# Performance work log

Hardware: AMD Instinct MI355X
Metric: run time of the kernel (lower is better)

## Reference

```python
import jax, jax.numpy as jnp
import numpy as np

PATCH = 16
B, C, H, W = 4, 3, 512, 512
N = 4096  # patches per image


def setup_inputs() -> dict:
    key = jax.random.key(0)
    k1, k2, k3, k4 = jax.random.split(key, 4)
    fuse = jax.random.normal(k1, (B, C, H, W), jnp.float32)
    img1 = jax.random.normal(k2, (B, C, H, W), jnp.float32)
    img2 = jax.random.normal(k3, (B, C, H, W), jnp.float32)
    # valid top-left (h, w) so h+PATCH <= H, w+PATCH <= W
    coords = jax.random.randint(k4, (B, N, 2), 0, H - PATCH + 1, dtype=jnp.int32)
    return {"fuse": fuse, "img1": img1, "img2": img2, "coords": coords}


def _extract_patches(image, coords):
    # image: [B,C,H,W], coords: [B,N,2] -> patches [B,C,N,P] with P=PATCH*PATCH
    c = image.shape[1]

    def one(img_b, hw):
        p = jax.lax.dynamic_slice(img_b, (0, hw[0], hw[1]), (c, PATCH, PATCH))
        return p.reshape(c, PATCH * PATCH)

    pat = jax.vmap(jax.vmap(one, in_axes=(None, 0)), in_axes=(0, 0))(image, coords)  # [B,N,C,P]
    return jnp.transpose(pat, (0, 2, 1, 3))  # [B,C,N,P]


def reference(fuse, img1, img2, coords):
    pf = _extract_patches(fuse, coords)
    p1 = _extract_patches(img1, coords)
    p2 = _extract_patches(img2, coords)
    mu1 = jnp.mean(p1, axis=-1, keepdims=True)
    mu2 = jnp.mean(p2, axis=-1, keepdims=True)
    sd1 = jnp.sqrt(jnp.mean((p1 - mu1) ** 2, axis=-1, keepdims=True))
    sd2 = jnp.sqrt(jnp.mean((p2 - mu2) ** 2, axis=-1, keepdims=True))
    denom = sd1 + sd2 + 1e-6
    target = (sd1 / denom) * p1 + (sd2 / denom) * p2
    return jnp.mean(jnp.abs(pf - target))
```

## Files before the change

kernel.cpp:

```cpp
#include <hip/hip_runtime.h>

#define BD 4
#define CD 3
#define HD 512
#define WD 512
#define NPAT 4096
#define NP (BD * NPAT)
#define PLANE (HD * WD)
#define PPW 2
#define PPB (PPW * 4)
#define NBLK (NP / PPB)
#define TOTAL_ELEMS (4.0 * 3.0 * 4096.0 * 256.0)
#define CSTRIDE 260

typedef float f4 __attribute__((ext_vector_type(4), aligned(4)));

template <int CTRL>
__device__ __forceinline__ float dpp_add(float x) {
    int y = __builtin_amdgcn_update_dpp(0, __float_as_int(x), CTRL, 0xF, 0xF, true);
    return x + __int_as_float(y);
}

__device__ __forceinline__ float wave_sum64(float x) {
    x = dpp_add<0xB1>(x);
    x = dpp_add<0x4E>(x);
    x = dpp_add<0x124>(x);
    x = dpp_add<0x128>(x);
    x += __shfl_xor(x, 16, 64);
    x += __shfl_xor(x, 32, 64);
    return x;
}

__global__ __launch_bounds__(256) void build_order(
    const int* __restrict__ coords, unsigned int* __restrict__ order)
{
    __shared__ unsigned char  cnt[256 * CSTRIDE];
    __shared__ unsigned short total[256];
    __shared__ unsigned int   base[256];

    const int t = threadIdx.x;
    const int b = blockIdx.x;

    {
        unsigned int* row = (unsigned int*)(cnt + t * CSTRIDE);
        #pragma unroll
        for (int k = 0; k < CSTRIDE / 4; ++k) row[k] = 0u;
    }
    __syncthreads();

    const int2* c2 = (const int2*)coords;
    unsigned int  pk[16];
    unsigned char kk[16];
    #pragma unroll
    for (int i = 0; i < 16; ++i) {
        const int p = (b << 12) + (i << 8) + t;
        const int2 hw = c2[p];
        pk[i] = ((unsigned)b << 18) | ((unsigned)hw.x << 9) | (unsigned)hw.y;
        kk[i] = (unsigned char)(((hw.x >> 5) << 4) | (hw.y >> 5));
        cnt[t * CSTRIDE + kk[i]]++;
    }
    __syncthreads();

    {
        unsigned int run = 0;
        for (int tt = 0; tt < 256; ++tt) {
            const unsigned int v = cnt[tt * CSTRIDE + t];
            cnt[tt * CSTRIDE + t] = (unsigned char)run;
            run += v;
        }
        total[t] = (unsigned short)run;
    }
    __syncthreads();

    if (t < 64) {
        const unsigned int t0 = total[4 * t],     t1 = total[4 * t + 1];
        const unsigned int t2 = total[4 * t + 2], t3 = total[4 * t + 3];
        const unsigned int lsum = t0 + t1 + t2 + t3;
        unsigned int x = lsum;
        #pragma unroll
        for (int d = 1; d < 64; d <<= 1) {
            const unsigned int v = __shfl_up(x, d, 64);
            if (t >= d) x += v;
        }
        const unsigned int excl = x - lsum;
        base[4 * t]     = excl;
        base[4 * t + 1] = excl + t0;
        base[4 * t + 2] = excl + t0 + t1;
        base[4 * t + 3] = excl + t0 + t1 + t2;
    }
    __syncthreads();

    #pragma unroll
    for (int i = 0; i < 16; ++i) {
        const int key = kk[i];
        const unsigned int pos = base[key] + cnt[t * CSTRIDE + key];
        cnt[t * CSTRIDE + key]++;
        order[(b << 12) + pos] = pk[i];
    }
}

__global__ __launch_bounds__(256) void patch_stage1(
    const float* __restrict__ fuse,
    const float* __restrict__ img1,
    const float* __restrict__ img2,
    const unsigned int* __restrict__ order,
    float* __restrict__ partials)
{
    const int lane = threadIdx.x & 63;
    const int wave = threadIdx.x >> 6;
    const int bid  = blockIdx.x;
    const int slot0 = (((bid & 7) * (NBLK / 8) + (bid >> 3)) << 3) + wave * PPW;

    const uint2 ord = *(const uint2*)(order + slot0);

    const int wA = ord.x & 511, hA = (ord.x >> 9) & 511, bA = ord.x >> 18;
    const int wB = ord.y & 511, hB = (ord.y >> 9) & 511, bB = ord.y >> 18;

    const int roff = (lane >> 2) * WD + (lane & 3) * 4;
    const size_t baseA = ((size_t)(bA * CD) * HD + hA) * WD + wA + roff;
    const size_t baseB = ((size_t)(bB * CD) * HD + hB) * WD + wB + roff;

    f4 vfA[3], v1A[3], v2A[3], vfB[3], v1B[3], v2B[3];
    #pragma unroll
    for (int c = 0; c < CD; ++c) {
        vfA[c] = *(const f4*)(fuse + baseA + (size_t)c * PLANE);
        v1A[c] = *(const f4*)(img1 + baseA + (size_t)c * PLANE);
        v2A[c] = *(const f4*)(img2 + baseA + (size_t)c * PLANE);
        vfB[c] = *(const f4*)(fuse + baseB + (size_t)c * PLANE);
        v1B[c] = *(const f4*)(img1 + baseB + (size_t)c * PLANE);
        v2B[c] = *(const f4*)(img2 + baseB + (size_t)c * PLANE);
    }

    float s1[2][3], q1[2][3], s2[2][3], q2[2][3];
    #pragma unroll
    for (int c = 0; c < CD; ++c) {
        s1[0][c] = v1A[c].x + v1A[c].y + v1A[c].z + v1A[c].w;
        q1[0][c] = v1A[c].x*v1A[c].x + v1A[c].y*v1A[c].y + v1A[c].z*v1A[c].z + v1A[c].w*v1A[c].w;
        s2[0][c] = v2A[c].x + v2A[c].y + v2A[c].z + v2A[c].w;
        q2[0][c] = v2A[c].x*v2A[c].x + v2A[c].y*v2A[c].y + v2A[c].z*v2A[c].z + v2A[c].w*v2A[c].w;
        s1[1][c] = v1B[c].x + v1B[c].y + v1B[c].z + v1B[c].w;
        q1[1][c] = v1B[c].x*v1B[c].x + v1B[c].y*v1B[c].y + v1B[c].z*v1B[c].z + v1B[c].w*v1B[c].w;
        s2[1][c] = v2B[c].x + v2B[c].y + v2B[c].z + v2B[c].w;
        q2[1][c] = v2B[c].x*v2B[c].x + v2B[c].y*v2B[c].y + v2B[c].z*v2B[c].z + v2B[c].w*v2B[c].w;
    }

    #pragma unroll
    for (int u = 0; u < 2; ++u) {
        #pragma unroll
        for (int c = 0; c < CD; ++c) {
            s1[u][c] = wave_sum64(s1[u][c]);
            q1[u][c] = wave_sum64(q1[u][c]);
            s2[u][c] = wave_sum64(s2[u][c]);
            q2[u][c] = wave_sum64(q2[u][c]);
        }
    }

    const float inv = 1.f / 256.f;
    float acc = 0.f;
    #pragma unroll
    for (int u = 0; u < 2; ++u) {
        #pragma unroll
        for (int c = 0; c < CD; ++c) {
            const float mu1 = s1[u][c] * inv;
            const float mu2 = s2[u][c] * inv;
            const float sd1 = sqrtf(fmaxf(q1[u][c] * inv - mu1 * mu1, 0.f));
            const float sd2 = sqrtf(fmaxf(q2[u][c] * inv - mu2 * mu2, 0.f));
            const float denom = sd1 + sd2 + 1e-6f;
            const float w1 = sd1 / denom;
            const float w2 = sd2 / denom;
            const f4 vf = u ? vfB[c] : vfA[c];
            const f4 v1 = u ? v1B[c] : v1A[c];
            const f4 v2 = u ? v2B[c] : v2A[c];
            acc += fabsf(vf.x - (w1 * v1.x + w2 * v2.x))
                 + fabsf(vf.y - (w1 * v1.y + w2 * v2.y))
                 + fabsf(vf.z - (w1 * v1.z + w2 * v2.z))
                 + fabsf(vf.w - (w1 * v1.w + w2 * v2.w));
        }
    }

    acc = wave_sum64(acc);

    __shared__ float partsm[4];
    if (lane == 0) partsm[wave] = acc;
    __syncthreads();
    if (threadIdx.x == 0)
        partials[bid] = partsm[0] + partsm[1] + partsm[2] + partsm[3];
}

__global__ __launch_bounds__(256) void patch_stage2(
    const float* __restrict__ partials, float* __restrict__ out)
{
    float s = 0.f;
    for (int i = threadIdx.x; i < NBLK; i += 256)
        s += partials[i];

    s = wave_sum64(s);

    __shared__ float partsm[4];
    const int lane = threadIdx.x & 63;
    const int wave = threadIdx.x >> 6;
    if (lane == 0) partsm[wave] = s;
    __syncthreads();
    if (threadIdx.x == 0)
        out[0] = (partsm[0] + partsm[1] + partsm[2] + partsm[3]) * (float)(1.0 / TOTAL_ELEMS);
}

extern "C" void kernel_launch(void* const* d_in, const int* in_sizes, int n_in,
                              void* d_out, int out_size, void* d_ws, size_t ws_size,
                              hipStream_t stream) {
    const float* fuse   = (const float*)d_in[0];
    const float* img1   = (const float*)d_in[1];
    const float* img2   = (const float*)d_in[2];
    const int*   coords = (const int*)d_in[3];
    float* out = (float*)d_out;

    unsigned int* order    = (unsigned int*)d_ws;
    float*        partials = (float*)((char*)d_ws + NP * 4);

    build_order<<<BD, 256, 0, stream>>>(coords, order);
    patch_stage1<<<NBLK, 256, 0, stream>>>(fuse, img1, img2, order, partials);
    patch_stage2<<<1, 256, 0, stream>>>(partials, out);
}
```

Before: 32.33 us.

## Make stage-1 blocks persistent over four iterations with double-buffered register prefetch

The grid for the patch statistics kernel shrinks from 2048 blocks to 512. Each block now loops over four groups of eight patches and issues the loads for the next group before computing the current one, using two register buffers. The aim is to hide global-load latency inside a block and to cut block launch and reduction overhead. In exchange, register pressure roughly doubles (the kernel asks for 2 blocks per SIMD via launch bounds), which lowers occupancy and could leave fewer waves to hide latency.

```diff
diff --git a/kernel.cpp b/kernel.cpp
--- a/kernel.cpp
+++ b/kernel.cpp
@@ -7,9 +7,8 @@
 #define NPAT 4096
 #define NP (BD * NPAT)
 #define PLANE (HD * WD)
-#define PPW 2
-#define PPB (PPW * 4)
-#define NBLK (NP / PPB)
+#define NBLK 512
+#define ITER 4
 #define TOTAL_ELEMS (4.0 * 3.0 * 4096.0 * 256.0)
 #define CSTRIDE 260
 
@@ -99,7 +98,7 @@
     }
 }
 
-__global__ __launch_bounds__(256) void patch_stage1(
+__global__ __launch_bounds__(256, 2) void patch_stage1(
     const float* __restrict__ fuse,
     const float* __restrict__ img1,
     const float* __restrict__ img2,
@@ -109,79 +108,86 @@
     const int lane = threadIdx.x & 63;
     const int wave = threadIdx.x >> 6;
     const int bid  = blockIdx.x;
-    const int slot0 = (((bid & 7) * (NBLK / 8) + (bid >> 3)) << 3) + wave * PPW;
-
-    const uint2 ord = *(const uint2*)(order + slot0);
-
-    const int wA = ord.x & 511, hA = (ord.x >> 9) & 511, bA = ord.x >> 18;
-    const int wB = ord.y & 511, hB = (ord.y >> 9) & 511, bB = ord.y >> 18;
-
+    const int S = ((bid & 7) * (NBLK / 8) + (bid >> 3)) * 32;
     const int roff = (lane >> 2) * WD + (lane & 3) * 4;
-    const size_t baseA = ((size_t)(bA * CD) * HD + hA) * WD + wA + roff;
-    const size_t baseB = ((size_t)(bB * CD) * HD + hB) * WD + wB + roff;
-
-    f4 vfA[3], v1A[3], v2A[3], vfB[3], v1B[3], v2B[3];
+
+    f4 buf[2][18];
+
+    #define ISSUE(j, bsel) do {                                               \
+        const uint2 o = *(const uint2*)(order + S + (j) * 8 + wave * 2);      \
+        const int wA = o.x & 511, hA = (o.x >> 9) & 511, bA = (int)(o.x >> 18);\
+        const int wB = o.y & 511, hB = (o.y >> 9) & 511, bB = (int)(o.y >> 18);\
+        const size_t baseA = ((size_t)(bA * CD) * HD + hA) * WD + wA + roff;  \
+        const size_t baseB = ((size_t)(bB * CD) * HD + hB) * WD + wB + roff;  \
+        _Pragma("unroll")                                                     \
+        for (int c = 0; c < CD; ++c) {                                        \
+            buf[bsel][c*6+0] = *(const f4*)(fuse + baseA + (size_t)c * PLANE);\
+            buf[bsel][c*6+1] = *(const f4*)(img1 + baseA + (size_t)c * PLANE);\
+            buf[bsel][c*6+2] = *(const f4*)(img2 + baseA + (size_t)c * PLANE);\
+            buf[bsel][c*6+3] = *(const f4*)(fuse + baseB + (size_t)c * PLANE);\
+            buf[bsel][c*6+4] = *(const f4*)(img1 + baseB + (size_t)c * PLANE);\
+            buf[bsel][c*6+5] = *(const f4*)(img2 + baseB + (size_t)c * PLANE);\
+        }                                                                     \
+    } while (0)
+
+    float accT = 0.f;
+    const float inv = 1.f / 256.f;
+
+    ISSUE(0, 0);
     #pragma unroll
-    for (int c = 0; c < CD; ++c) {
-        vfA[c] = *(const f4*)(fuse + baseA + (size_t)c * PLANE);
-        v1A[c] = *(const f4*)(img1 + baseA + (size_t)c * PLANE);
-        v2A[c] = *(const f4*)(img2 + baseA + (size_t)c * PLANE);
-        vfB[c] = *(const f4*)(fuse + baseB + (size_t)c * PLANE);
-        v1B[c] = *(const f4*)(img1 + baseB + (size_t)c * PLANE);
-        v2B[c] = *(const f4*)(img2 + baseB + (size_t)c * PLANE);
-    }
-
-    float s1[2][3], q1[2][3], s2[2][3], q2[2][3];
-    #pragma unroll
-    for (int c = 0; c < CD; ++c) {
-        s1[0][c] = v1A[c].x + v1A[c].y + v1A[c].z + v1A[c].w;
-        q1[0][c] = v1A[c].x*v1A[c].x + v1A[c].y*v1A[c].y + v1A[c].z*v1A[c].z + v1A[c].w*v1A[c].w;
-        s2[0][c] = v2A[c].x + v2A[c].y + v2A[c].z + v2A[c].w;
-        q2[0][c] = v2A[c].x*v2A[c].x + v2A[c].y*v2A[c].y + v2A[c].z*v2A[c].z + v2A[c].w*v2A[c].w;
-        s1[1][c] = v1B[c].x + v1B[c].y + v1B[c].z + v1B[c].w;
-        q1[1][c] = v1B[c].x*v1B[c].x + v1B[c].y*v1B[c].y + v1B[c].z*v1B[c].z + v1B[c].w*v1B[c].w;
-        s2[1][c] = v2B[c].x + v2B[c].y + v2B[c].z + v2B[c].w;
-        q2[1][c] = v2B[c].x*v2B[c].x + v2B[c].y*v2B[c].y + v2B[c].z*v2B[c].z + v2B[c].w*v2B[c].w;
-    }
-
-    #pragma unroll
-    for (int u = 0; u < 2; ++u) {
-        #pragma unroll
-        for (int c = 0; c < CD; ++c) {
-            s1[u][c] = wave_sum64(s1[u][c]);
-            q1[u][c] = wave_sum64(q1[u][c]);
-            s2[u][c] = wave_sum64(s2[u][c]);
-            q2[u][c] = wave_sum64(q2[u][c]);
+    for (int j = 0; j < ITER; ++j) {
+        if (j < ITER - 1) ISSUE(j + 1, (j + 1) & 1);
+
+        {
+            float s1[2][3], q1[2][3], s2[2][3], q2[2][3];
+            #pragma unroll
+            for (int u = 0; u < 2; ++u) {
+                #pragma unroll
+                for (int c = 0; c < CD; ++c) {
+                    const f4 a  = buf[j & 1][c*6 + u*3 + 1];
+                    const f4 bb = buf[j & 1][c*6 + u*3 + 2];
+                    s1[u][c] = a.x + a.y + a.z + a.w;
+                    q1[u][c] = a.x*a.x + a.y*a.y + a.z*a.z + a.w*a.w;
+                    s2[u][c] = bb.x + bb.y + bb.z + bb.w;
+                    q2[u][c] = bb.x*bb.x + bb.y*bb.y + bb.z*bb.z + bb.w*bb.w;
+                }
+            }
+            #pragma unroll
+            for (int u = 0; u < 2; ++u) {
+                #pragma unroll
+                for (int c = 0; c < CD; ++c) {
+                    s1[u][c] = wave_sum64(s1[u][c]);
+                    q1[u][c] = wave_sum64(q1[u][c]);
+                    s2[u][c] = wave_sum64(s2[u][c]);
+                    q2[u][c] = wave_sum64(q2[u][c]);
+                }
+            }
+            #pragma unroll
+            for (int u = 0; u < 2; ++u) {
+                #pragma unroll
+                for (int c = 0; c < CD; ++c) {
+                    const float mu1 = s1[u][c] * inv;
+                    const float mu2 = s2[u][c] * inv;
+                    const float sd1 = sqrtf(fmaxf(q1[u][c] * inv - mu1 * mu1, 0.f));
+                    const float sd2 = sqrtf(fmaxf(q2[u][c] * inv - mu2 * mu2, 0.f));
+                    const float den = sd1 + sd2 + 1e-6f;
+                    const float w1 = sd1 / den;
+                    const float w2 = sd2 / den;
+                    const f4 vf = buf[j & 1][c*6 + u*3 + 0];
+                    const f4 a  = buf[j & 1][c*6 + u*3 + 1];
+                    const f4 bb = buf[j & 1][c*6 + u*3 + 2];
+                    const f4 d0 = vf - (w1 * a + w2 * bb);
+                    accT += (fabsf(d0.x) + fabsf(d0.y)) + (fabsf(d0.z) + fabsf(d0.w));
+                }
+            }
         }
     }
-
-    const float inv = 1.f / 256.f;
-    float acc = 0.f;
-    #pragma unroll
-    for (int u = 0; u < 2; ++u) {
-        #pragma unroll
-        for (int c = 0; c < CD; ++c) {
-            const float mu1 = s1[u][c] * inv;
-            const float mu2 = s2[u][c] * inv;
-            const float sd1 = sqrtf(fmaxf(q1[u][c] * inv - mu1 * mu1, 0.f));
-            const float sd2 = sqrtf(fmaxf(q2[u][c] * inv - mu2 * mu2, 0.f));
-            const float denom = sd1 + sd2 + 1e-6f;
-            const float w1 = sd1 / denom;
-            const float w2 = sd2 / denom;
-            const f4 vf = u ? vfB[c] : vfA[c];
-            const f4 v1 = u ? v1B[c] : v1A[c];
-            const f4 v2 = u ? v2B[c] : v2A[c];
-            acc += fabsf(vf.x - (w1 * v1.x + w2 * v2.x))
-                 + fabsf(vf.y - (w1 * v1.y + w2 * v2.y))
-                 + fabsf(vf.z - (w1 * v1.z + w2 * v2.z))
-                 + fabsf(vf.w - (w1 * v1.w + w2 * v2.w));
-        }
-    }
-
-    acc = wave_sum64(acc);
+    #undef ISSUE
+
+    accT = wave_sum64(accT);
 
     __shared__ float partsm[4];
-    if (lane == 0) partsm[wave] = acc;
+    if (lane == 0) partsm[wave] = accT;
     __syncthreads();
     if (threadIdx.x == 0)
         partials[bid] = partsm[0] + partsm[1] + partsm[2] + partsm[3];
```

After: 33.41 us. +3.3%, slower.

## Stage 32x32 image bins in LDS and process all bin patches per block

Applied to the files above, without the earlier changes.

Each block now owns one 32x32 coordinate bin (plus a 15-pixel halo), loads that region of all three images channel by channel into shared memory, and then evaluates every patch in the bin from LDS. build_order additionally emits per-bin start and count arrays. Overlapping patches therefore reuse staged data instead of each patch re-reading global memory. The wave reduction also switches from shfl_xor to row-broadcast DPP plus readlane. In exchange, load across blocks becomes uneven with per-bin counts, and blocks now make serialized per-channel passes separated by barriers.

```diff
diff --git a/kernel.cpp b/kernel.cpp
--- a/kernel.cpp
+++ b/kernel.cpp
@@ -7,9 +7,8 @@
 #define NPAT 4096
 #define NP (BD * NPAT)
 #define PLANE (HD * WD)
-#define PPW 2
-#define PPB (PPW * 4)
-#define NBLK (NP / PPB)
+#define GRID1 1024
+#define SROW 51
 #define TOTAL_ELEMS (4.0 * 3.0 * 4096.0 * 256.0)
 #define CSTRIDE 260
 
@@ -21,18 +20,19 @@
     return x + __int_as_float(y);
 }
 
-__device__ __forceinline__ float wave_sum64(float x) {
+__device__ __forceinline__ float wave_total(float x) {
     x = dpp_add<0xB1>(x);
     x = dpp_add<0x4E>(x);
     x = dpp_add<0x124>(x);
     x = dpp_add<0x128>(x);
-    x += __shfl_xor(x, 16, 64);
-    x += __shfl_xor(x, 32, 64);
-    return x;
+    x = dpp_add<0x142>(x);
+    x = dpp_add<0x143>(x);
+    return __int_as_float(__builtin_amdgcn_readlane(__float_as_int(x), 63));
 }
 
 __global__ __launch_bounds__(256) void build_order(
-    const int* __restrict__ coords, unsigned int* __restrict__ order)
+    const int* __restrict__ coords, unsigned int* __restrict__ order,
+    unsigned int* __restrict__ starts, unsigned int* __restrict__ counts)
 {
     __shared__ unsigned char  cnt[256 * CSTRIDE];
     __shared__ unsigned short total[256];
@@ -90,6 +90,9 @@
     }
     __syncthreads();
 
+    starts[(b << 8) + t] = (unsigned)(b << 12) + base[t];
+    counts[(b << 8) + t] = total[t];
+
     #pragma unroll
     for (int i = 0; i < 16; ++i) {
         const int key = kk[i];
@@ -104,86 +107,90 @@
     const float* __restrict__ img1,
     const float* __restrict__ img2,
     const unsigned int* __restrict__ order,
+    const unsigned int* __restrict__ starts,
+    const unsigned int* __restrict__ counts,
     float* __restrict__ partials)
 {
-    const int lane = threadIdx.x & 63;
-    const int wave = threadIdx.x >> 6;
+    const int tid  = threadIdx.x;
+    const int lane = tid & 63;
+    const int wave = tid >> 6;
     const int bid  = blockIdx.x;
-    const int slot0 = (((bid & 7) * (NBLK / 8) + (bid >> 3)) << 3) + wave * PPW;
-
-    const uint2 ord = *(const uint2*)(order + slot0);
-
-    const int wA = ord.x & 511, hA = (ord.x >> 9) & 511, bA = ord.x >> 18;
-    const int wB = ord.y & 511, hB = (ord.y >> 9) & 511, bB = ord.y >> 18;
-
-    const int roff = (lane >> 2) * WD + (lane & 3) * 4;
-    const size_t baseA = ((size_t)(bA * CD) * HD + hA) * WD + wA + roff;
-    const size_t baseB = ((size_t)(bB * CD) * HD + hB) * WD + wB + roff;
-
-    f4 vfA[3], v1A[3], v2A[3], vfB[3], v1B[3], v2B[3];
-    #pragma unroll
+    const int sb  = (bid & 7) * (GRID1 / 8) + (bid >> 3);
+    const int b   = sb >> 8;
+    const int key = sb & 255;
+    const int kh  = key >> 4, kw = key & 15;
+
+    const unsigned s = starts[sb];
+    const int      n = (int)counts[sb];
+
+    __shared__ float slab[3][47 * SROW];
+    __shared__ float partsm[4];
+
+    if (n == 0) { if (tid == 0) partials[bid] = 0.f; return; }
+
+    const int R  = (kh == 15) ? 32 : 47;
+    const int C4 = (kw == 15) ? 8  : 12;
+    const float* const imgs[3] = { fuse, img1, img2 };
+
+    float accT = 0.f;
+    const float inv = 1.f / 256.f;
+
     for (int c = 0; c < CD; ++c) {
-        vfA[c] = *(const f4*)(fuse + baseA + (size_t)c * PLANE);
-        v1A[c] = *(const f4*)(img1 + baseA + (size_t)c * PLANE);
-        v2A[c] = *(const f4*)(img2 + baseA + (size_t)c * PLANE);
-        vfB[c] = *(const f4*)(fuse + baseB + (size_t)c * PLANE);
-        v1B[c] = *(const f4*)(img1 + baseB + (size_t)c * PLANE);
-        v2B[c] = *(const f4*)(img2 + baseB + (size_t)c * PLANE);
-    }
-
-    float s1[2][3], q1[2][3], s2[2][3], q2[2][3];
-    #pragma unroll
-    for (int c = 0; c < CD; ++c) {
-        s1[0][c] = v1A[c].x + v1A[c].y + v1A[c].z + v1A[c].w;
-        q1[0][c] = v1A[c].x*v1A[c].x + v1A[c].y*v1A[c].y + v1A[c].z*v1A[c].z + v1A[c].w*v1A[c].w;
-        s2[0][c] = v2A[c].x + v2A[c].y + v2A[c].z + v2A[c].w;
-        q2[0][c] = v2A[c].x*v2A[c].x + v2A[c].y*v2A[c].y + v2A[c].z*v2A[c].z + v2A[c].w*v2A[c].w;
-        s1[1][c] = v1B[c].x + v1B[c].y + v1B[c].z + v1B[c].w;
-        q1[1][c] = v1B[c].x*v1B[c].x + v1B[c].y*v1B[c].y + v1B[c].z*v1B[c].z + v1B[c].w*v1B[c].w;
-        s2[1][c] = v2B[c].x + v2B[c].y + v2B[c].z + v2B[c].w;
-        q2[1][c] = v2B[c].x*v2B[c].x + v2B[c].y*v2B[c].y + v2B[c].z*v2B[c].z + v2B[c].w*v2B[c].w;
-    }
-
-    #pragma unroll
-    for (int u = 0; u < 2; ++u) {
         #pragma unroll
-        for (int c = 0; c < CD; ++c) {
-            s1[u][c] = wave_sum64(s1[u][c]);
-            q1[u][c] = wave_sum64(q1[u][c]);
-            s2[u][c] = wave_sum64(s2[u][c]);
-            q2[u][c] = wave_sum64(q2[u][c]);
-        }
-    }
-
-    const float inv = 1.f / 256.f;
-    float acc = 0.f;
-    #pragma unroll
-    for (int u = 0; u < 2; ++u) {
-        #pragma unroll
-        for (int c = 0; c < CD; ++c) {
-            const float mu1 = s1[u][c] * inv;
-            const float mu2 = s2[u][c] * inv;
-            const float sd1 = sqrtf(fmaxf(q1[u][c] * inv - mu1 * mu1, 0.f));
-            const float sd2 = sqrtf(fmaxf(q2[u][c] * inv - mu2 * mu2, 0.f));
-            const float denom = sd1 + sd2 + 1e-6f;
-            const float w1 = sd1 / denom;
-            const float w2 = sd2 / denom;
-            const f4 vf = u ? vfB[c] : vfA[c];
-            const f4 v1 = u ? v1B[c] : v1A[c];
-            const f4 v2 = u ? v2B[c] : v2A[c];
-            acc += fabsf(vf.x - (w1 * v1.x + w2 * v2.x))
-                 + fabsf(vf.y - (w1 * v1.y + w2 * v2.y))
-                 + fabsf(vf.z - (w1 * v1.z + w2 * v2.z))
-                 + fabsf(vf.w - (w1 * v1.w + w2 * v2.w));
-        }
-    }
-
-    acc = wave_sum64(acc);
-
-    __shared__ float partsm[4];
-    if (lane == 0) partsm[wave] = acc;
-    __syncthreads();
-    if (threadIdx.x == 0)
+        for (int im = 0; im < 3; ++im) {
+            const float* gp = imgs[im]
+                + ((size_t)(b * CD + c) * HD + 32 * kh) * WD + 32 * kw;
+            for (int i = tid; i < R * 12; i += 256) {
+                const int r = i / 12;
+                const int k = i - r * 12;
+                if (k < C4) {
+                    const f4 v = *(const f4*)(gp + (size_t)r * WD + 4 * k);
+                    const int o = r * SROW + 4 * k;
+                    slab[im][o]     = v.x;
+                    slab[im][o + 1] = v.y;
+                    slab[im][o + 2] = v.z;
+                    slab[im][o + 3] = v.w;
+                }
+            }
+        }
+        __syncthreads();
+
+        for (int i = wave; i < n; i += 4) {
+            const unsigned o = order[s + i];
+            const int w0 = (int)(o & 511)        - 32 * kw;
+            const int h0 = (int)((o >> 9) & 511) - 32 * kh;
+            const int base = (h0 + (lane >> 2)) * SROW + w0 + (lane & 3) * 4;
+
+            const float a0 = slab[1][base],     a1 = slab[1][base + 1];
+            const float a2 = slab[1][base + 2], a3 = slab[1][base + 3];
+            const float b0 = slab[2][base],     b1 = slab[2][base + 1];
+            const float b2 = slab[2][base + 2], b3 = slab[2][base + 3];
+            const float f0 = slab[0][base],     f1 = slab[0][base + 1];
+            const float f2 = slab[0][base + 2], f3 = slab[0][base + 3];
+
+            const float s1 = wave_total((a0 + a1) + (a2 + a3));
+            const float q1 = wave_total((a0 * a0 + a1 * a1) + (a2 * a2 + a3 * a3));
+            const float s2 = wave_total((b0 + b1) + (b2 + b3));
+            const float q2 = wave_total((b0 * b0 + b1 * b1) + (b2 * b2 + b3 * b3));
+
+            const float mu1 = s1 * inv, mu2 = s2 * inv;
+            const float sd1 = sqrtf(fmaxf(q1 * inv - mu1 * mu1, 0.f));
+            const float sd2 = sqrtf(fmaxf(q2 * inv - mu2 * mu2, 0.f));
+            const float den = sd1 + sd2 + 1e-6f;
+            const float w1 = sd1 / den, w2 = sd2 / den;
+
+            accT += fabsf(f0 - (w1 * a0 + w2 * b0))
+                  + fabsf(f1 - (w1 * a1 + w2 * b1))
+                  + fabsf(f2 - (w1 * a2 + w2 * b2))
+                  + fabsf(f3 - (w1 * a3 + w2 * b3));
+        }
+        __syncthreads();
+    }
+
+    const float tot = wave_total(accT);
+    if (lane == 0) partsm[wave] = tot;
+    __syncthreads();
+    if (tid == 0)
         partials[bid] = partsm[0] + partsm[1] + partsm[2] + partsm[3];
 }
 
@@ -191,10 +198,10 @@
     const float* __restrict__ partials, float* __restrict__ out)
 {
     float s = 0.f;
-    for (int i = threadIdx.x; i < NBLK; i += 256)
+    for (int i = threadIdx.x; i < GRID1; i += 256)
         s += partials[i];
 
-    s = wave_sum64(s);
+    s = wave_total(s);
 
     __shared__ float partsm[4];
     const int lane = threadIdx.x & 63;
@@ -215,9 +222,12 @@
     float* out = (float*)d_out;
 
     unsigned int* order    = (unsigned int*)d_ws;
-    float*        partials = (float*)((char*)d_ws + NP * 4);
-
-    build_order<<<BD, 256, 0, stream>>>(coords, order);
-    patch_stage1<<<NBLK, 256, 0, stream>>>(fuse, img1, img2, order, partials);
+    unsigned int* starts   = order + NP;
+    unsigned int* counts   = starts + GRID1;
+    float*        partials = (float*)(counts + GRID1);
+
+    build_order<<<BD, 256, 0, stream>>>(coords, order, starts, counts);
+    patch_stage1<<<GRID1, 256, 0, stream>>>(fuse, img1, img2, order,
+                                            starts, counts, partials);
     patch_stage2<<<1, 256, 0, stream>>>(partials, out);
 }
```

Result: slower. 42.67 us (+32.0%).
